# Optimization experiments

Measured on AMD Instinct MI355X. Metric: run time of the kernel, lower is better.

## Reference

```python
import jax, jax.numpy as jnp
import numpy as np

EPS = 1e-6

def rms_norm(x):
    # RMSNorm over last dim, no learned weight (torch F.rms_norm without weight)
    return x * jax.lax.rsqrt(jnp.mean(jnp.square(x), axis=-1, keepdims=True) + EPS)

def apply_rotary_emb(x, cos, sin):
    # x: [b, t, h, d]; cos/sin: [t, d//2] -> broadcast [1, t, 1, d//2]
    half = x.shape[-1] // 2
    c = cos[None, :, None, :]
    s = sin[None, :, None, :]
    x1, x2 = x[..., :half], x[..., half:]
    return jnp.concatenate([x1 * c - x2 * s, x2 * c + x1 * s], axis=-1)

def setup_inputs() -> dict:
    key = jax.random.key(0)
    ks = jax.random.split(key, 16)
    B, T, E, H = 4, 2048, 1024, 16
    D = E // H
    inp = {
        "query": jax.random.normal(ks[0], (B, T, E), jnp.float32),
        "key": jax.random.normal(ks[1], (B, T, E), jnp.float32),
        "value": jax.random.normal(ks[2], (B, T, E), jnp.float32),
        "attn_mask": jnp.tril(jnp.ones((T, T), dtype=bool)),
        "cos": jnp.cos(jnp.arange(T)[:, None] / (10000.0 ** (jnp.arange(D // 2) / (D // 2)))[None, :]).astype(jnp.float32),
        "sin": jnp.sin(jnp.arange(T)[:, None] / (10000.0 ** (jnp.arange(D // 2) / (D // 2)))[None, :]).astype(jnp.float32),
        "Wq": jax.random.normal(ks[3], (E, E), jnp.float32) * 0.02,
        "bq": jnp.zeros((E,), jnp.float32),
        "Wk": jax.random.normal(ks[4], (E, E), jnp.float32) * 0.02,
        "bk": jnp.zeros((E,), jnp.float32),
        "Wv": jax.random.normal(ks[5], (E, E), jnp.float32) * 0.02,
        "bv": jnp.zeros((E,), jnp.float32),
        "Wo": jax.random.normal(ks[6], (E, E), jnp.float32) * 0.02,
        "bo": jnp.zeros((E,), jnp.float32),
    }
    return inp

def reference(query, key, value, attn_mask, cos, sin, Wq, bq, Wk, bk, Wv, bv, Wo, bo):
    B, T, E = query.shape
    H = 16
    D = E // H
    q = query @ Wq.T + bq
    k = key @ Wk.T + bk
    v = value @ Wv.T + bv
    q = q.reshape(B, T, H, D)
    k = k.reshape(B, T, H, D)
    v = v.reshape(B, T, H, D)
    q, k = rms_norm(q), rms_norm(k)
    q = apply_rotary_emb(q, cos, sin)
    k = apply_rotary_emb(k, cos, sin)
    # SDPA: [b, h, t, d] layout via einsum directly from [b, t, h, d]
    scale = 1.0 / jnp.sqrt(jnp.float32(D))
    scores = jnp.einsum('bqhd,bkhd->bhqk', q, k) * scale
    scores = jnp.where(attn_mask[None, None, :, :], scores, jnp.float32(-jnp.inf))
    attn = jax.nn.softmax(scores, axis=-1)
    o = jnp.einsum('bhqk,bkhd->bqhd', attn, v).reshape(B, T, E)
    return o @ Wo.T + bo
```

## Files before the change

### kernel.cpp

```cpp
#include <hip/hip_runtime.h>

typedef __bf16 bf16;
typedef __bf16 bf16x8 __attribute__((ext_vector_type(8)));
typedef __bf16 bf16x4 __attribute__((ext_vector_type(4)));
typedef float  floatx4 __attribute__((ext_vector_type(4)));

#define B_ 4
#define T_ 2048
#define E_ 1024
#define H_ 16
#define D_ 64
#define NTE_ (B_ * T_ * E_)

#define NEG_BIG (-1e30f)
#define SMAX2 12.2629081f

#define OFF_CQ 0ull
#define OFF_CK ((unsigned long long)NTE_)
#define OFF_CV (2ull * NTE_)
#define OFF_WQ (3ull * NTE_)
#define OFF_WK (OFF_WQ + 1048576ull)
#define OFF_WV (OFF_WK + 1048576ull)
#define OFF_WO (OFF_WV + 1048576ull)
__device__ bf16 g_conv[3ull * NTE_ + 4ull * 1048576ull];
__device__ bf16 g_scratch[5ull * NTE_];

__device__ __forceinline__ floatx4 mfma16(bf16x8 a, bf16x8 b, floatx4 c) {
  return __builtin_amdgcn_mfma_f32_16x16x32_bf16(a, b, c, 0, 0, 0);
}

__device__ __forceinline__ void async_copy16(void* lds, const void* g) {
  __builtin_amdgcn_global_load_lds(
      (const __attribute__((address_space(1))) unsigned int*)g,
      (__attribute__((address_space(3))) unsigned int*)lds, 16, 0, 0);
}

__global__ __launch_bounds__(256) void convert_all(const float4* __restrict__ q,
                                                   const float4* __restrict__ k,
                                                   const float4* __restrict__ v,
                                                   const float4* __restrict__ wq,
                                                   const float4* __restrict__ wk,
                                                   const float4* __restrict__ wv,
                                                   const float4* __restrict__ wo) {
  const float4* srcs[7] = {q, k, v, wq, wk, wv, wo};
  bf16x4* dsts[7] = {(bf16x4*)(g_conv + OFF_CQ), (bf16x4*)(g_conv + OFF_CK),
                     (bf16x4*)(g_conv + OFF_CV), (bf16x4*)(g_conv + OFF_WQ),
                     (bf16x4*)(g_conv + OFF_WK), (bf16x4*)(g_conv + OFF_WV),
                     (bf16x4*)(g_conv + OFF_WO)};
  const int n4s[7] = {NTE_ / 4, NTE_ / 4, NTE_ / 4, 262144, 262144, 262144, 262144};
  int i0 = blockIdx.x * 256 + threadIdx.x;
  int stride = gridDim.x * 256;
#pragma unroll
  for (int s = 0; s < 7; ++s) {
    const float4* sp = srcs[s];
    bf16x4* dp = dsts[s];
    int n4 = n4s[s];
    for (int i = i0; i < n4; i += stride) {
      float4 vv = sp[i];
      bf16x4 o;
      o[0] = (bf16)vv.x; o[1] = (bf16)vv.y; o[2] = (bf16)vv.z; o[3] = (bf16)vv.w;
      dp[i] = o;
    }
  }
}

template <bool OUTF32>
__device__ __forceinline__ void gemm256_core(const bf16* __restrict__ X,
                                             const bf16* __restrict__ W,
                                             const float* __restrict__ bias,
                                             void* __restrict__ Yv,
                                             int M0, int N0) {
  constexpr int NT = 16;
  __shared__ __align__(16) char smem[131072];

  const int tid = threadIdx.x;
  const int w = tid >> 6;
  const int l = tid & 63;
  const int q = l >> 4;
  const int r = l & 15;
  const int lrow = l >> 3;
  const int qxr = q ^ (r & 7);
  const int so0 = qxr << 4;
  const int so1 = so0 ^ 64;
  const int colb = ((l & 7) ^ lrow) << 4;

  const int wm = (w >> 2) * 128;
  const int wn = (w & 3) * 64;
  const int halfA = w >> 2;
  const int halfB = (w & 3) >> 1;

  char* const sm = smem;
  const char* const rdA = sm + halfA * 16384 + r * 128;
  const char* const rdB = sm + 32768 + halfB * 16384 + ((w & 1) * 64 + r) * 128;
  char* const stA = sm + w * 1024;
  char* const stB = sm + 32768 + w * 1024;

  const char* const gA = (const char*)X + ((size_t)(M0 + w * 8 + lrow)) * 2048 + colb;
  const char* const gB = (const char*)W + ((size_t)(N0 + w * 8 + lrow)) * 2048 + colb;

  floatx4 acc[8][4];
#pragma unroll
  for (int mi = 0; mi < 8; ++mi)
#pragma unroll
    for (int ni = 0; ni < 4; ++ni) acc[mi][ni] = (floatx4){0.f, 0.f, 0.f, 0.f};

#define ST_A(p, h, t)                                          \
  do {                                                         \
    char* d_ = stA + (p) * 65536 + (h) * 16384;                \
    const char* s_ = gA + (size_t)(h) * (128 * 2048) + (t) * 128; \
    async_copy16(d_, s_);                                      \
    async_copy16(d_ + 8192, s_ + 64 * 2048);                   \
  } while (0)
#define ST_B(p, h, t)                                          \
  do {                                                         \
    char* d_ = stB + (p) * 65536 + (h) * 16384;                \
    const char* s_ = gB + (size_t)(h) * (128 * 2048) + (t) * 128; \
    async_copy16(d_, s_);                                      \
    async_copy16(d_ + 8192, s_ + 64 * 2048);                   \
  } while (0)

  ST_B(0, 0, 0); ST_B(0, 1, 0); ST_A(0, 0, 0); ST_A(0, 1, 0);
  ST_B(1, 0, 1); ST_B(1, 1, 1); ST_A(1, 0, 1); ST_A(1, 1, 1);
  asm volatile("s_waitcnt vmcnt(8)" ::: "memory");
  __builtin_amdgcn_s_barrier();

  bf16x8 aR[4][2], b0[2][2], b1[2][2];

#pragma unroll 2
  for (int t = 0; t < NT; ++t) {
    const int p = t & 1;
    const char* rA = rdA + p * 65536;
    const char* rB = rdB + p * 65536;

#pragma unroll
    for (int mi = 0; mi < 4; ++mi) {
      aR[mi][0] = *(const bf16x8*)(rA + mi * 2048 + so0);
      aR[mi][1] = *(const bf16x8*)(rA + mi * 2048 + so1);
    }
#pragma unroll
    for (int ni = 0; ni < 2; ++ni) {
      b0[ni][0] = *(const bf16x8*)(rB + ni * 2048 + so0);
      b0[ni][1] = *(const bf16x8*)(rB + ni * 2048 + so1);
    }
    __builtin_amdgcn_s_barrier();
    asm volatile("s_waitcnt lgkmcnt(0)" ::: "memory");
    __builtin_amdgcn_sched_barrier(0);
    __builtin_amdgcn_s_setprio(1);
#pragma unroll
    for (int mi = 0; mi < 4; ++mi)
#pragma unroll
      for (int ni = 0; ni < 2; ++ni) {
        acc[mi][ni] = mfma16(aR[mi][0], b0[ni][0], acc[mi][ni]);
        acc[mi][ni] = mfma16(aR[mi][1], b0[ni][1], acc[mi][ni]);
      }
    __builtin_amdgcn_s_setprio(0);
    __builtin_amdgcn_s_barrier();

#pragma unroll
    for (int ni = 0; ni < 2; ++ni) {
      b1[ni][0] = *(const bf16x8*)(rB + (ni + 2) * 2048 + so0);
      b1[ni][1] = *(const bf16x8*)(rB + (ni + 2) * 2048 + so1);
    }
    __builtin_amdgcn_s_barrier();
    asm volatile("s_waitcnt lgkmcnt(0)" ::: "memory");
    __builtin_amdgcn_sched_barrier(0);
    __builtin_amdgcn_s_setprio(1);
#pragma unroll
    for (int mi = 0; mi < 4; ++mi)
#pragma unroll
      for (int ni = 0; ni < 2; ++ni) {
        acc[mi][ni + 2] = mfma16(aR[mi][0], b1[ni][0], acc[mi][ni + 2]);
        acc[mi][ni + 2] = mfma16(aR[mi][1], b1[ni][1], acc[mi][ni + 2]);
      }
    __builtin_amdgcn_s_setprio(0);
    __builtin_amdgcn_s_barrier();

#pragma unroll
    for (int mi = 0; mi < 4; ++mi) {
      aR[mi][0] = *(const bf16x8*)(rA + 8192 + mi * 2048 + so0);
      aR[mi][1] = *(const bf16x8*)(rA + 8192 + mi * 2048 + so1);
    }
    if (t + 2 < NT) { ST_B(p, 0, t + 2); ST_B(p, 1, t + 2); }
    __builtin_amdgcn_s_barrier();
    asm volatile("s_waitcnt lgkmcnt(0)" ::: "memory");
    __builtin_amdgcn_sched_barrier(0);
    __builtin_amdgcn_s_setprio(1);
#pragma unroll
    for (int mi = 0; mi < 4; ++mi)
#pragma unroll
      for (int ni = 0; ni < 2; ++ni) {
        acc[mi + 4][ni + 2] = mfma16(aR[mi][0], b1[ni][0], acc[mi + 4][ni + 2]);
        acc[mi + 4][ni + 2] = mfma16(aR[mi][1], b1[ni][1], acc[mi + 4][ni + 2]);
      }
    __builtin_amdgcn_s_setprio(0);
    __builtin_amdgcn_s_barrier();

    if (t + 2 < NT) { ST_A(p, 0, t + 2); ST_A(p, 1, t + 2); }
    __builtin_amdgcn_s_barrier();
    __builtin_amdgcn_s_setprio(1);
#pragma unroll
    for (int mi = 0; mi < 4; ++mi)
#pragma unroll
      for (int ni = 0; ni < 2; ++ni) {
        acc[mi + 4][ni] = mfma16(aR[mi][0], b0[ni][0], acc[mi + 4][ni]);
        acc[mi + 4][ni] = mfma16(aR[mi][1], b0[ni][1], acc[mi + 4][ni]);
      }
    __builtin_amdgcn_s_setprio(0);
    if (t + 2 < NT) {
      asm volatile("s_waitcnt vmcnt(8)" ::: "memory");
    } else {
      asm volatile("s_waitcnt vmcnt(0)" ::: "memory");
    }
    __builtin_amdgcn_s_barrier();
  }
#undef ST_A
#undef ST_B

  float bvv[4];
#pragma unroll
  for (int ni = 0; ni < 4; ++ni) bvv[ni] = bias[N0 + wn + ni * 16 + r];

  if (OUTF32) {
    float* Y = (float*)Yv;
#pragma unroll
    for (int mi = 0; mi < 8; ++mi) {
      int rowbase = M0 + wm + mi * 16 + q * 4;
#pragma unroll
      for (int ni = 0; ni < 4; ++ni) {
        int col = N0 + wn + ni * 16 + r;
#pragma unroll
        for (int rr = 0; rr < 4; ++rr)
          Y[(size_t)(rowbase + rr) * 1024 + col] = acc[mi][ni][rr] + bvv[ni];
      }
    }
  } else {
    bf16* Y = (bf16*)Yv;
#pragma unroll
    for (int mi = 0; mi < 8; ++mi) {
      int rowbase = M0 + wm + mi * 16 + q * 4;
#pragma unroll
      for (int ni = 0; ni < 4; ++ni) {
        int col = N0 + wn + ni * 16 + r;
#pragma unroll
        for (int rr = 0; rr < 4; ++rr)
          Y[(size_t)(rowbase + rr) * 1024 + col] = (bf16)(acc[mi][ni][rr] + bvv[ni]);
      }
    }
  }
}

__global__ __launch_bounds__(512, 2) void gemm_qkv(const float* __restrict__ bq,
                                                   const float* __restrict__ bk,
                                                   const float* __restrict__ bv) {
  int bid = blockIdx.x;
  int s = (bid & 7) * 48 + (bid >> 3);
  int z = s >> 7;
  int rm = s & 127;
  int mt = rm >> 2, nt = rm & 3;
  const bf16* X = g_conv + OFF_CQ + (unsigned long long)z * NTE_;
  const bf16* W = g_conv + OFF_WQ + (unsigned long long)z * 1048576ull;
  const float* bias = (z == 0) ? bq : (z == 1) ? bk : bv;
  bf16* Y = g_scratch + (unsigned long long)z * NTE_;
  gemm256_core<false>(X, W, bias, (void*)Y, mt * 256, nt * 256);
}

__global__ __launch_bounds__(512, 2) void gemm_out(const bf16* __restrict__ X,
                                                   const bf16* __restrict__ W,
                                                   const float* __restrict__ bias,
                                                   float* __restrict__ Y) {
  int bid = blockIdx.x;
  int s = (bid & 7) * 16 + (bid >> 3);
  int mt = s >> 2, nt = s & 3;
  gemm256_core<true>(X, W, bias, (void*)Y, mt * 256, nt * 256);
}

__global__ __launch_bounds__(256) void rmsnorm_rope(const float* __restrict__ cosb,
                                                    const float* __restrict__ sinb) {
  bf16* qp = g_scratch;
  bf16* kp = g_scratch + (unsigned long long)NTE_;
  constexpr int HR = B_ * T_ * H_;
  int gid = blockIdx.x * 16 + (threadIdx.x >> 4);
  int j = threadIdx.x & 15;
  bool isq = (gid < HR);
  bf16* base = isq ? qp : kp;
  float post = isq ? 0.18033688f : 1.0f;
  int row = gid & (HR - 1);
  int t = (row >> 4) & (T_ - 1);
  bf16* p = base + (size_t)row * 64 + j * 4;

  bf16x4 xv = *(const bf16x4*)p;
  float x[4], ss = 0.f;
#pragma unroll
  for (int i = 0; i < 4; ++i) { x[i] = (float)xv[i]; ss += x[i] * x[i]; }
#pragma unroll
  for (int m = 1; m < 16; m <<= 1) ss += __shfl_xor(ss, m, 64);
  float rs = rsqrtf(ss * (1.0f / 64.0f) + 1e-6f);

  float y[4], pr[4];
#pragma unroll
  for (int i = 0; i < 4; ++i) y[i] = x[i] * rs;
#pragma unroll
  for (int i = 0; i < 4; ++i) pr[i] = __shfl_xor(y[i], 8, 64);

  int dbase = (j & 7) * 4;
  bf16x4 ov;
#pragma unroll
  for (int i = 0; i < 4; ++i) {
    float c = cosb[t * 32 + dbase + i];
    float s = sinb[t * 32 + dbase + i];
    float o = (j < 8) ? (y[i] * c - pr[i] * s) : (y[i] * c + pr[i] * s);
    ov[i] = (bf16)(o * post);
  }
  *(bf16x4*)p = ov;
}

__global__ __launch_bounds__(256) void transpose_v() {
  const bf16* vp = g_scratch + 2ull * NTE_;
  bf16* vt = g_scratch + 3ull * NTE_;
  __shared__ bf16 tile[64][72];
  int bid = blockIdx.x;
  int tt = bid & 31;
  int bh = bid >> 5;
  int h = bh & 15, b = bh >> 4;
  int t0 = tt * 64;
  int tid = threadIdx.x;
#pragma unroll
  for (int i = 0; i < 2; ++i) {
    int idx = i * 256 + tid;
    int row = idx >> 3, cc = (idx & 7) * 8;
    bf16x8 v = *(const bf16x8*)(vp + (size_t)(b * T_ + t0 + row) * E_ + h * D_ + cc);
#pragma unroll
    for (int jj = 0; jj < 8; ++jj) tile[row][cc + jj] = v[jj];
  }
  __syncthreads();
#pragma unroll
  for (int i = 0; i < 2; ++i) {
    int idx = i * 256 + tid;
    int d = idx >> 3, tc = (idx & 7) * 8;
    bf16x8 v;
#pragma unroll
    for (int jj = 0; jj < 8; ++jj) v[jj] = tile[tc + jj][d];
    *(bf16x8*)(vt + ((size_t)bh * D_ + d) * T_ + t0 + tc) = v;
  }
}

#define KSTR 72
#define PSTR 72
__global__ __launch_bounds__(256, 4) void flash_attn() {
  const bf16* qp = g_scratch;
  const bf16* kp = g_scratch + (unsigned long long)NTE_;
  const bf16* vt = g_scratch + 3ull * NTE_;
  bf16* op = g_scratch + 4ull * NTE_;

  __shared__ __align__(16) bf16 sK[64 * KSTR];
  __shared__ __align__(16) bf16 sV[64 * KSTR];
  __shared__ __align__(16) bf16 sP[4 * 32 * PSTR];

  const int bid = blockIdx.x;
  const int xcd = bid & 7;
  const int lb = bid >> 3;
  const int bh = xcd * 8 + (lb & 7);
  const int qt = 15 - (lb >> 3);
  const int h = bh & 15, b = bh >> 4;
  const int tid = threadIdx.x, w = tid >> 6, l = tid & 63, g = l >> 4, r = l & 15;
  const int Q0 = qt * 128;
  const int qw = Q0 + w * 32;

  const bf16* kbase = kp + (size_t)(b * T_) * E_ + h * D_;
  const bf16* vbase = vt + (size_t)bh * D_ * T_;
  bf16* pw = sP + w * (32 * PSTR);

  bf16x8 ones;
#pragma unroll
  for (int i = 0; i < 8; ++i) ones[i] = (bf16)1.0f;

  bf16x8 qa[2][2];
#pragma unroll
  for (int qb = 0; qb < 2; ++qb)
#pragma unroll
    for (int hf = 0; hf < 2; ++hf)
      qa[qb][hf] = *(const bf16x8*)(qp + (size_t)(b * T_ + qw + qb * 16 + r) * E_ +
                                    h * D_ + hf * 32 + g * 8);

  floatx4 o_acc[2][4], l_acc[2];
#pragma unroll
  for (int qb = 0; qb < 2; ++qb) {
    l_acc[qb] = (floatx4){0.f, 0.f, 0.f, 0.f};
#pragma unroll
    for (int dt = 0; dt < 4; ++dt) o_acc[qb][dt] = (floatx4){0.f, 0.f, 0.f, 0.f};
  }

  int srow[2], scc[2];
#pragma unroll
  for (int i = 0; i < 2; ++i) {
    int idx = i * 256 + tid;
    srow[i] = idx >> 3;
    scc[i] = (idx & 7) * 8;
  }

  bf16x8 kreg[2], vreg[2];
#pragma unroll
  for (int i = 0; i < 2; ++i) {
    kreg[i] = *(const bf16x8*)(kbase + (size_t)srow[i] * E_ + scc[i]);
    vreg[i] = *(const bf16x8*)(vbase + (size_t)srow[i] * T_ + scc[i]);
  }

  const int lastKt = Q0 + 64;
  for (int kt0 = 0; kt0 <= lastKt; kt0 += 64) {
    __syncthreads();
#pragma unroll
    for (int i = 0; i < 2; ++i) {
      *(bf16x8*)(sK + srow[i] * KSTR + scc[i]) = kreg[i];
      *(bf16x8*)(sV + srow[i] * KSTR + scc[i]) = vreg[i];
    }
    if (kt0 < lastKt) {
      int kt1 = kt0 + 64;
#pragma unroll
      for (int i = 0; i < 2; ++i) {
        kreg[i] = *(const bf16x8*)(kbase + (size_t)(kt1 + srow[i]) * E_ + scc[i]);
        vreg[i] = *(const bf16x8*)(vbase + (size_t)srow[i] * T_ + kt1 + scc[i]);
      }
    }
    __syncthreads();

    if (kt0 <= qw + 31) {
      const bool needMask = (kt0 + 63 > qw);

#pragma unroll
      for (int sc = 0; sc < 4; ++sc) {
        bf16x8 kb0 = *(const bf16x8*)(sK + (sc * 16 + r) * KSTR + g * 8);
        bf16x8 kb1 = *(const bf16x8*)(sK + (sc * 16 + r) * KSTR + 32 + g * 8);
        floatx4 s0 = (floatx4){0.f, 0.f, 0.f, 0.f};
        floatx4 s1 = (floatx4){0.f, 0.f, 0.f, 0.f};
        s0 = mfma16(kb0, qa[0][0], s0);
        s0 = mfma16(kb1, qa[0][1], s0);
        s1 = mfma16(kb0, qa[1][0], s1);
        s1 = mfma16(kb1, qa[1][1], s1);

        if (needMask) {
          int kg = kt0 + sc * 16 + g * 4;
          int qg0 = qw + r;
          int qg1 = qw + 16 + r;
#pragma unroll
          for (int rr = 0; rr < 4; ++rr) {
            if (kg + rr > qg0) s0[rr] = NEG_BIG;
            if (kg + rr > qg1) s1[rr] = NEG_BIG;
          }
        }

        bf16x4 p0, p1;
#pragma unroll
        for (int rr = 0; rr < 4; ++rr) {
          p0[rr] = (bf16)exp2f(s0[rr] - SMAX2);
          p1[rr] = (bf16)exp2f(s1[rr] - SMAX2);
        }
        *(bf16x4*)(pw + r * PSTR + sc * 16 + g * 4) = p0;
        *(bf16x4*)(pw + (16 + r) * PSTR + sc * 16 + g * 4) = p1;
      }

#pragma unroll
      for (int kk = 0; kk < 2; ++kk) {
        bf16x8 vb[4];
#pragma unroll
        for (int dt = 0; dt < 4; ++dt)
          vb[dt] = *(const bf16x8*)(sV + (dt * 16 + r) * KSTR + kk * 32 + g * 8);
#pragma unroll
        for (int qb = 0; qb < 2; ++qb) {
          bf16x8 pa = *(const bf16x8*)(pw + (qb * 16 + r) * PSTR + kk * 32 + g * 8);
          l_acc[qb] = mfma16(pa, ones, l_acc[qb]);
#pragma unroll
          for (int dt = 0; dt < 4; ++dt)
            o_acc[qb][dt] = mfma16(pa, vb[dt], o_acc[qb][dt]);
        }
      }
    }
  }

  float linv[2][4];
#pragma unroll
  for (int qb = 0; qb < 2; ++qb)
#pragma unroll
    for (int rr = 0; rr < 4; ++rr) linv[qb][rr] = 1.0f / l_acc[qb][rr];
#pragma unroll
  for (int qb = 0; qb < 2; ++qb)
#pragma unroll
    for (int dt = 0; dt < 4; ++dt)
#pragma unroll
      for (int rr = 0; rr < 4; ++rr) {
        int t = qw + qb * 16 + g * 4 + rr;
        op[(size_t)(b * T_ + t) * E_ + h * D_ + dt * 16 + r] =
            (bf16)(o_acc[qb][dt][rr] * linv[qb][rr]);
      }
}

extern "C" void kernel_launch(void* const* d_in, const int* in_sizes, int n_in,
                              void* d_out, int out_size, void* d_ws, size_t ws_size,
                              hipStream_t stream) {
  float* out = (float*)d_out;

  void* cvp_ = nullptr;
  void* sp_ = nullptr;
  hipGetSymbolAddress(&cvp_, HIP_SYMBOL(g_conv));
  hipGetSymbolAddress(&sp_, HIP_SYMBOL(g_scratch));
  bf16* cv = (bf16*)cvp_;
  bf16* sc = (bf16*)sp_;

  const float* cosb = (const float*)d_in[4];
  const float* sinb = (const float*)d_in[5];
  const float* bq = (const float*)d_in[7];
  const float* bk = (const float*)d_in[9];
  const float* bv = (const float*)d_in[11];
  const float* bo = (const float*)d_in[13];

  convert_all<<<dim3(1024), dim3(256), 0, stream>>>(
      (const float4*)d_in[0], (const float4*)d_in[1], (const float4*)d_in[2],
      (const float4*)d_in[6], (const float4*)d_in[8], (const float4*)d_in[10],
      (const float4*)d_in[12]);

  bf16* op = sc + 4ull * NTE_;

  gemm_qkv<<<dim3(384), dim3(512), 0, stream>>>(bq, bk, bv);
  rmsnorm_rope<<<dim3(16384), dim3(256), 0, stream>>>(cosb, sinb);
  transpose_v<<<dim3(2048), dim3(256), 0, stream>>>();
  flash_attn<<<dim3(1024), dim3(256), 0, stream>>>();
  gemm_out<<<dim3(128), dim3(512), 0, stream>>>(op, cv + OFF_WO, bo, out);
}
```

Before: 372.4 us.

## Fuse RMSNorm, RoPE and V transpose into GEMM epilogues; shrink GEMM tile to 128x256

The QKV GEMM now applies RMSNorm, rotary embedding and the q scale directly in its epilogue, and writes V already transposed into the [b,h,d,t] layout. This removes the separate rmsnorm_rope and transpose_v kernels along with their global memory round trips. The GEMM tile is reduced from 256x256 to 128x256 with a restructured double-buffered LDS schedule and one block per CU, which doubles the grid for better CU coverage. The cost is more B-tile reloads per output and scattered 2-byte stores in the fused epilogue.

```diff
diff --git a/kernel.cpp b/kernel.cpp
--- a/kernel.cpp
+++ b/kernel.cpp
@@ -64,14 +64,15 @@
   }
 }
 
-template <bool OUTF32>
-__device__ __forceinline__ void gemm256_core(const bf16* __restrict__ X,
-                                             const bf16* __restrict__ W,
-                                             const float* __restrict__ bias,
-                                             void* __restrict__ Yv,
-                                             int M0, int N0) {
+template <int EPI>
+__device__ __forceinline__ void gemm_core(char* __restrict__ smem,
+                                          const bf16* __restrict__ X,
+                                          const bf16* __restrict__ W,
+                                          const float* __restrict__ bias,
+                                          void* __restrict__ Yv, int M0, int N0,
+                                          const float* __restrict__ cosb,
+                                          const float* __restrict__ sinb) {
   constexpr int NT = 16;
-  __shared__ __align__(16) char smem[131072];
 
   const int tid = threadIdx.x;
   const int w = tid >> 6;
@@ -79,69 +80,68 @@
   const int q = l >> 4;
   const int r = l & 15;
   const int lrow = l >> 3;
-  const int qxr = q ^ (r & 7);
-  const int so0 = qxr << 4;
-  const int so1 = so0 ^ 64;
+  const int rs7 = r & 7;
+  const int wm = (w >> 2) * 64;
+  const int wn = (w & 3) * 64;
   const int colb = ((l & 7) ^ lrow) << 4;
-
-  const int wm = (w >> 2) * 128;
-  const int wn = (w & 3) * 64;
-  const int halfA = w >> 2;
-  const int halfB = (w & 3) >> 1;
-
-  char* const sm = smem;
-  const char* const rdA = sm + halfA * 16384 + r * 128;
-  const char* const rdB = sm + 32768 + halfB * 16384 + ((w & 1) * 64 + r) * 128;
-  char* const stA = sm + w * 1024;
-  char* const stB = sm + 32768 + w * 1024;
-
-  const char* const gA = (const char*)X + ((size_t)(M0 + w * 8 + lrow)) * 2048 + colb;
-  const char* const gB = (const char*)W + ((size_t)(N0 + w * 8 + lrow)) * 2048 + colb;
-
-  floatx4 acc[8][4];
-#pragma unroll
-  for (int mi = 0; mi < 8; ++mi)
+  const int sl0 = ((0 + q) ^ rs7) << 4;
+  const int sl1 = ((4 + q) ^ rs7) << 4;
+
+  char* const Ab = smem;
+  char* const Bb = smem + 32768;
+  const int aoff = (wm + r) * 128;
+  const int boff = (wn + r) * 128;
+
+  const char* gA = (const char*)X + (size_t)(M0 + w * 16 + lrow) * 2048 + colb;
+  const char* gB = (const char*)W + (size_t)(N0 + w * 32 + lrow) * 2048 + colb;
+
+  floatx4 acc[4][4];
+#pragma unroll
+  for (int mi = 0; mi < 4; ++mi)
 #pragma unroll
     for (int ni = 0; ni < 4; ++ni) acc[mi][ni] = (floatx4){0.f, 0.f, 0.f, 0.f};
 
-#define ST_A(p, h, t)                                          \
+#define STA(p, t)                                              \
   do {                                                         \
-    char* d_ = stA + (p) * 65536 + (h) * 16384;                \
-    const char* s_ = gA + (size_t)(h) * (128 * 2048) + (t) * 128; \
+    char* d_ = Ab + (p) * 16384 + w * 2048;                    \
+    const char* s_ = gA + (size_t)(t) * 128;                   \
     async_copy16(d_, s_);                                      \
-    async_copy16(d_ + 8192, s_ + 64 * 2048);                   \
+    async_copy16(d_ + 1024, s_ + 16384);                       \
   } while (0)
-#define ST_B(p, h, t)                                          \
+#define STB(p, t)                                              \
   do {                                                         \
-    char* d_ = stB + (p) * 65536 + (h) * 16384;                \
-    const char* s_ = gB + (size_t)(h) * (128 * 2048) + (t) * 128; \
+    char* d_ = Bb + (p) * 32768 + w * 4096;                    \
+    const char* s_ = gB + (size_t)(t) * 128;                   \
     async_copy16(d_, s_);                                      \
-    async_copy16(d_ + 8192, s_ + 64 * 2048);                   \
+    async_copy16(d_ + 1024, s_ + 16384);                       \
+    async_copy16(d_ + 2048, s_ + 32768);                       \
+    async_copy16(d_ + 3072, s_ + 49152);                       \
   } while (0)
 
-  ST_B(0, 0, 0); ST_B(0, 1, 0); ST_A(0, 0, 0); ST_A(0, 1, 0);
-  ST_B(1, 0, 1); ST_B(1, 1, 1); ST_A(1, 0, 1); ST_A(1, 1, 1);
-  asm volatile("s_waitcnt vmcnt(8)" ::: "memory");
+  STB(0, 0); STA(0, 0);
+  STB(1, 1); STA(1, 1);
+  asm volatile("s_waitcnt vmcnt(6)" ::: "memory");
   __builtin_amdgcn_s_barrier();
 
-  bf16x8 aR[4][2], b0[2][2], b1[2][2];
+  bf16x8 af[4][2], bf0[2][2], bf1[2][2];
 
 #pragma unroll 2
   for (int t = 0; t < NT; ++t) {
     const int p = t & 1;
-    const char* rA = rdA + p * 65536;
-    const char* rB = rdB + p * 65536;
+    const char* rA = Ab + p * 16384;
+    const char* rB = Bb + p * 32768;
 
 #pragma unroll
     for (int mi = 0; mi < 4; ++mi) {
-      aR[mi][0] = *(const bf16x8*)(rA + mi * 2048 + so0);
-      aR[mi][1] = *(const bf16x8*)(rA + mi * 2048 + so1);
+      af[mi][0] = *(const bf16x8*)(rA + aoff + mi * 2048 + sl0);
+      af[mi][1] = *(const bf16x8*)(rA + aoff + mi * 2048 + sl1);
     }
 #pragma unroll
     for (int ni = 0; ni < 2; ++ni) {
-      b0[ni][0] = *(const bf16x8*)(rB + ni * 2048 + so0);
-      b0[ni][1] = *(const bf16x8*)(rB + ni * 2048 + so1);
-    }
+      bf0[ni][0] = *(const bf16x8*)(rB + boff + ni * 2048 + sl0);
+      bf0[ni][1] = *(const bf16x8*)(rB + boff + ni * 2048 + sl1);
+    }
+    if (t >= 1 && t + 1 < NT) { STB(p ^ 1, t + 1); }
     __builtin_amdgcn_s_barrier();
     asm volatile("s_waitcnt lgkmcnt(0)" ::: "memory");
     __builtin_amdgcn_sched_barrier(0);
@@ -150,17 +150,18 @@
     for (int mi = 0; mi < 4; ++mi)
 #pragma unroll
       for (int ni = 0; ni < 2; ++ni) {
-        acc[mi][ni] = mfma16(aR[mi][0], b0[ni][0], acc[mi][ni]);
-        acc[mi][ni] = mfma16(aR[mi][1], b0[ni][1], acc[mi][ni]);
+        acc[mi][ni] = mfma16(af[mi][0], bf0[ni][0], acc[mi][ni]);
+        acc[mi][ni] = mfma16(af[mi][1], bf0[ni][1], acc[mi][ni]);
       }
     __builtin_amdgcn_s_setprio(0);
     __builtin_amdgcn_s_barrier();
 
 #pragma unroll
     for (int ni = 0; ni < 2; ++ni) {
-      b1[ni][0] = *(const bf16x8*)(rB + (ni + 2) * 2048 + so0);
-      b1[ni][1] = *(const bf16x8*)(rB + (ni + 2) * 2048 + so1);
-    }
+      bf1[ni][0] = *(const bf16x8*)(rB + boff + (ni + 2) * 2048 + sl0);
+      bf1[ni][1] = *(const bf16x8*)(rB + boff + (ni + 2) * 2048 + sl1);
+    }
+    if (t + 2 < NT) { STA(p, t + 2); }
     __builtin_amdgcn_s_barrier();
     asm volatile("s_waitcnt lgkmcnt(0)" ::: "memory");
     __builtin_amdgcn_sched_barrier(0);
@@ -169,179 +170,122 @@
     for (int mi = 0; mi < 4; ++mi)
 #pragma unroll
       for (int ni = 0; ni < 2; ++ni) {
-        acc[mi][ni + 2] = mfma16(aR[mi][0], b1[ni][0], acc[mi][ni + 2]);
-        acc[mi][ni + 2] = mfma16(aR[mi][1], b1[ni][1], acc[mi][ni + 2]);
-      }
-    __builtin_amdgcn_s_setprio(0);
-    __builtin_amdgcn_s_barrier();
-
-#pragma unroll
-    for (int mi = 0; mi < 4; ++mi) {
-      aR[mi][0] = *(const bf16x8*)(rA + 8192 + mi * 2048 + so0);
-      aR[mi][1] = *(const bf16x8*)(rA + 8192 + mi * 2048 + so1);
-    }
-    if (t + 2 < NT) { ST_B(p, 0, t + 2); ST_B(p, 1, t + 2); }
-    __builtin_amdgcn_s_barrier();
-    asm volatile("s_waitcnt lgkmcnt(0)" ::: "memory");
-    __builtin_amdgcn_sched_barrier(0);
-    __builtin_amdgcn_s_setprio(1);
-#pragma unroll
-    for (int mi = 0; mi < 4; ++mi)
-#pragma unroll
-      for (int ni = 0; ni < 2; ++ni) {
-        acc[mi + 4][ni + 2] = mfma16(aR[mi][0], b1[ni][0], acc[mi + 4][ni + 2]);
-        acc[mi + 4][ni + 2] = mfma16(aR[mi][1], b1[ni][1], acc[mi + 4][ni + 2]);
-      }
-    __builtin_amdgcn_s_setprio(0);
-    __builtin_amdgcn_s_barrier();
-
-    if (t + 2 < NT) { ST_A(p, 0, t + 2); ST_A(p, 1, t + 2); }
-    __builtin_amdgcn_s_barrier();
-    __builtin_amdgcn_s_setprio(1);
-#pragma unroll
-    for (int mi = 0; mi < 4; ++mi)
-#pragma unroll
-      for (int ni = 0; ni < 2; ++ni) {
-        acc[mi + 4][ni] = mfma16(aR[mi][0], b0[ni][0], acc[mi + 4][ni]);
-        acc[mi + 4][ni] = mfma16(aR[mi][1], b0[ni][1], acc[mi + 4][ni]);
+        acc[mi][ni + 2] = mfma16(af[mi][0], bf1[ni][0], acc[mi][ni + 2]);
+        acc[mi][ni + 2] = mfma16(af[mi][1], bf1[ni][1], acc[mi][ni + 2]);
       }
     __builtin_amdgcn_s_setprio(0);
     if (t + 2 < NT) {
-      asm volatile("s_waitcnt vmcnt(8)" ::: "memory");
-    } else {
+      asm volatile("s_waitcnt vmcnt(2)" ::: "memory");
+    } else if (t + 1 < NT) {
       asm volatile("s_waitcnt vmcnt(0)" ::: "memory");
     }
     __builtin_amdgcn_s_barrier();
   }
-#undef ST_A
-#undef ST_B
-
-  float bvv[4];
-#pragma unroll
-  for (int ni = 0; ni < 4; ++ni) bvv[ni] = bias[N0 + wn + ni * 16 + r];
-
-  if (OUTF32) {
+#undef STA
+#undef STB
+
+  float bcol[4];
+#pragma unroll
+  for (int ni = 0; ni < 4; ++ni) bcol[ni] = bias[N0 + wn + ni * 16 + r];
+
+  if (EPI == 0 || EPI == 1) {
+    const float post = (EPI == 0) ? 0.18033688f : 1.0f;
+    bf16* Y = (bf16*)Yv;
+#pragma unroll
+    for (int mi = 0; mi < 4; ++mi) {
+      const int rowbase = M0 + wm + mi * 16 + q * 4;
+#pragma unroll
+      for (int rr = 0; rr < 4; ++rr) {
+        const int row = rowbase + rr;
+        const int ts = row & (T_ - 1);
+        float v0 = acc[mi][0][rr] + bcol[0];
+        float v1 = acc[mi][1][rr] + bcol[1];
+        float v2 = acc[mi][2][rr] + bcol[2];
+        float v3 = acc[mi][3][rr] + bcol[3];
+        float ss = v0 * v0 + v1 * v1 + v2 * v2 + v3 * v3;
+        ss += __shfl_xor(ss, 1, 64);
+        ss += __shfl_xor(ss, 2, 64);
+        ss += __shfl_xor(ss, 4, 64);
+        ss += __shfl_xor(ss, 8, 64);
+        const float rs = rsqrtf(ss * (1.0f / 64.0f) + 1e-6f);
+        const float y0 = v0 * rs, y1 = v1 * rs, y2 = v2 * rs, y3 = v3 * rs;
+        const float c0 = cosb[ts * 32 + r], s0 = sinb[ts * 32 + r];
+        const float c1 = cosb[ts * 32 + 16 + r], s1 = sinb[ts * 32 + 16 + r];
+        bf16 o0 = (bf16)((y0 * c0 - y2 * s0) * post);
+        bf16 o1 = (bf16)((y1 * c1 - y3 * s1) * post);
+        bf16 o2 = (bf16)((y2 * c0 + y0 * s0) * post);
+        bf16 o3 = (bf16)((y3 * c1 + y1 * s1) * post);
+        bf16* yp = Y + (size_t)row * 1024 + N0 + wn + r;
+        yp[0] = o0; yp[16] = o1; yp[32] = o2; yp[48] = o3;
+      }
+    }
+  } else if (EPI == 2) {
+    bf16* Y = (bf16*)Yv;
+#pragma unroll
+    for (int mi = 0; mi < 4; ++mi) {
+      const int rowbase = M0 + wm + mi * 16 + q * 4;
+      const int bb = rowbase >> 11;
+      const int t0 = rowbase & (T_ - 1);
+#pragma unroll
+      for (int ni = 0; ni < 4; ++ni) {
+        const int col = N0 + wn + ni * 16 + r;
+        const int head = col >> 6;
+        const int d = col & 63;
+        bf16x4 pk;
+#pragma unroll
+        for (int rr = 0; rr < 4; ++rr) pk[rr] = (bf16)(acc[mi][ni][rr] + bcol[ni]);
+        *(bf16x4*)(Y + ((size_t)(bb * 16 + head) * 64 + d) * 2048 + t0) = pk;
+      }
+    }
+  } else {
     float* Y = (float*)Yv;
 #pragma unroll
-    for (int mi = 0; mi < 8; ++mi) {
-      int rowbase = M0 + wm + mi * 16 + q * 4;
+    for (int mi = 0; mi < 4; ++mi) {
+      const int rowbase = M0 + wm + mi * 16 + q * 4;
 #pragma unroll
       for (int ni = 0; ni < 4; ++ni) {
-        int col = N0 + wn + ni * 16 + r;
+        const int col = N0 + wn + ni * 16 + r;
 #pragma unroll
         for (int rr = 0; rr < 4; ++rr)
-          Y[(size_t)(rowbase + rr) * 1024 + col] = acc[mi][ni][rr] + bvv[ni];
-      }
-    }
-  } else {
-    bf16* Y = (bf16*)Yv;
-#pragma unroll
-    for (int mi = 0; mi < 8; ++mi) {
-      int rowbase = M0 + wm + mi * 16 + q * 4;
-#pragma unroll
-      for (int ni = 0; ni < 4; ++ni) {
-        int col = N0 + wn + ni * 16 + r;
-#pragma unroll
-        for (int rr = 0; rr < 4; ++rr)
-          Y[(size_t)(rowbase + rr) * 1024 + col] = (bf16)(acc[mi][ni][rr] + bvv[ni]);
-      }
-    }
-  }
-}
-
-__global__ __launch_bounds__(512, 2) void gemm_qkv(const float* __restrict__ bq,
+          Y[(size_t)(rowbase + rr) * 1024 + col] = acc[mi][ni][rr] + bcol[ni];
+      }
+    }
+  }
+}
+
+__global__ __launch_bounds__(512, 1) void gemm_qkv(const float* __restrict__ bq,
                                                    const float* __restrict__ bk,
-                                                   const float* __restrict__ bv) {
+                                                   const float* __restrict__ bv,
+                                                   const float* __restrict__ cosb,
+                                                   const float* __restrict__ sinb) {
+  __shared__ __align__(16) char smem[98304];
   int bid = blockIdx.x;
-  int s = (bid & 7) * 48 + (bid >> 3);
-  int z = s >> 7;
-  int rm = s & 127;
-  int mt = rm >> 2, nt = rm & 3;
+  int s = (bid & 7) * 96 + (bid >> 3);
+  int z = s >> 8;
+  int rem = s & 255;
+  int mt = rem >> 2, nt = rem & 3;
   const bf16* X = g_conv + OFF_CQ + (unsigned long long)z * NTE_;
   const bf16* W = g_conv + OFF_WQ + (unsigned long long)z * 1048576ull;
-  const float* bias = (z == 0) ? bq : (z == 1) ? bk : bv;
-  bf16* Y = g_scratch + (unsigned long long)z * NTE_;
-  gemm256_core<false>(X, W, bias, (void*)Y, mt * 256, nt * 256);
-}
-
-__global__ __launch_bounds__(512, 2) void gemm_out(const bf16* __restrict__ X,
+  if (z == 0) {
+    gemm_core<0>(smem, X, W, bq, (void*)g_scratch, mt * 128, nt * 256, cosb, sinb);
+  } else if (z == 1) {
+    gemm_core<1>(smem, X, W, bk, (void*)(g_scratch + (unsigned long long)NTE_),
+                 mt * 128, nt * 256, cosb, sinb);
+  } else {
+    gemm_core<2>(smem, X, W, bv, (void*)(g_scratch + 3ull * NTE_),
+                 mt * 128, nt * 256, nullptr, nullptr);
+  }
+}
+
+__global__ __launch_bounds__(512, 1) void gemm_out(const bf16* __restrict__ X,
                                                    const bf16* __restrict__ W,
                                                    const float* __restrict__ bias,
                                                    float* __restrict__ Y) {
+  __shared__ __align__(16) char smem[98304];
   int bid = blockIdx.x;
-  int s = (bid & 7) * 16 + (bid >> 3);
+  int s = (bid & 7) * 32 + (bid >> 3);
   int mt = s >> 2, nt = s & 3;
-  gemm256_core<true>(X, W, bias, (void*)Y, mt * 256, nt * 256);
-}
-
-__global__ __launch_bounds__(256) void rmsnorm_rope(const float* __restrict__ cosb,
-                                                    const float* __restrict__ sinb) {
-  bf16* qp = g_scratch;
-  bf16* kp = g_scratch + (unsigned long long)NTE_;
-  constexpr int HR = B_ * T_ * H_;
-  int gid = blockIdx.x * 16 + (threadIdx.x >> 4);
-  int j = threadIdx.x & 15;
-  bool isq = (gid < HR);
-  bf16* base = isq ? qp : kp;
-  float post = isq ? 0.18033688f : 1.0f;
-  int row = gid & (HR - 1);
-  int t = (row >> 4) & (T_ - 1);
-  bf16* p = base + (size_t)row * 64 + j * 4;
-
-  bf16x4 xv = *(const bf16x4*)p;
-  float x[4], ss = 0.f;
-#pragma unroll
-  for (int i = 0; i < 4; ++i) { x[i] = (float)xv[i]; ss += x[i] * x[i]; }
-#pragma unroll
-  for (int m = 1; m < 16; m <<= 1) ss += __shfl_xor(ss, m, 64);
-  float rs = rsqrtf(ss * (1.0f / 64.0f) + 1e-6f);
-
-  float y[4], pr[4];
-#pragma unroll
-  for (int i = 0; i < 4; ++i) y[i] = x[i] * rs;
-#pragma unroll
-  for (int i = 0; i < 4; ++i) pr[i] = __shfl_xor(y[i], 8, 64);
-
-  int dbase = (j & 7) * 4;
-  bf16x4 ov;
-#pragma unroll
-  for (int i = 0; i < 4; ++i) {
-    float c = cosb[t * 32 + dbase + i];
-    float s = sinb[t * 32 + dbase + i];
-    float o = (j < 8) ? (y[i] * c - pr[i] * s) : (y[i] * c + pr[i] * s);
-    ov[i] = (bf16)(o * post);
-  }
-  *(bf16x4*)p = ov;
-}
-
-__global__ __launch_bounds__(256) void transpose_v() {
-  const bf16* vp = g_scratch + 2ull * NTE_;
-  bf16* vt = g_scratch + 3ull * NTE_;
-  __shared__ bf16 tile[64][72];
-  int bid = blockIdx.x;
-  int tt = bid & 31;
-  int bh = bid >> 5;
-  int h = bh & 15, b = bh >> 4;
-  int t0 = tt * 64;
-  int tid = threadIdx.x;
-#pragma unroll
-  for (int i = 0; i < 2; ++i) {
-    int idx = i * 256 + tid;
-    int row = idx >> 3, cc = (idx & 7) * 8;
-    bf16x8 v = *(const bf16x8*)(vp + (size_t)(b * T_ + t0 + row) * E_ + h * D_ + cc);
-#pragma unroll
-    for (int jj = 0; jj < 8; ++jj) tile[row][cc + jj] = v[jj];
-  }
-  __syncthreads();
-#pragma unroll
-  for (int i = 0; i < 2; ++i) {
-    int idx = i * 256 + tid;
-    int d = idx >> 3, tc = (idx & 7) * 8;
-    bf16x8 v;
-#pragma unroll
-    for (int jj = 0; jj < 8; ++jj) v[jj] = tile[tc + jj][d];
-    *(bf16x8*)(vt + ((size_t)bh * D_ + d) * T_ + t0 + tc) = v;
-  }
+  gemm_core<3>(smem, X, W, bias, (void*)Y, mt * 128, nt * 256, nullptr, nullptr);
 }
 
 #define KSTR 72
@@ -500,8 +444,8 @@
 
   void* cvp_ = nullptr;
   void* sp_ = nullptr;
-  hipGetSymbolAddress(&cvp_, HIP_SYMBOL(g_conv));
-  hipGetSymbolAddress(&sp_, HIP_SYMBOL(g_scratch));
+  (void)hipGetSymbolAddress(&cvp_, HIP_SYMBOL(g_conv));
+  (void)hipGetSymbolAddress(&sp_, HIP_SYMBOL(g_scratch));
   bf16* cv = (bf16*)cvp_;
   bf16* sc = (bf16*)sp_;
 
@@ -519,9 +463,7 @@
 
   bf16* op = sc + 4ull * NTE_;
 
-  gemm_qkv<<<dim3(384), dim3(512), 0, stream>>>(bq, bk, bv);
-  rmsnorm_rope<<<dim3(16384), dim3(256), 0, stream>>>(cosb, sinb);
-  transpose_v<<<dim3(2048), dim3(256), 0, stream>>>();
+  gemm_qkv<<<dim3(768), dim3(512), 0, stream>>>(bq, bk, bv, cosb, sinb);
   flash_attn<<<dim3(1024), dim3(256), 0, stream>>>();
-  gemm_out<<<dim3(128), dim3(512), 0, stream>>>(op, cv + OFF_WO, bo, out);
-}
+  gemm_out<<<dim3(256), dim3(512), 0, stream>>>(op, cv + OFF_WO, bo, out);
+}
```

Result: faster. 327.6 us (-12.0%).
